# Performance work log

Hardware: AMD Instinct MI355X
Metric: run time of the kernel (lower is better)

Reference implementation:

```python
import jax, jax.numpy as jnp
import numpy as np

N_EVENTS = 16
N_SAMPLES = 2 ** 15          # 32768
STEP = 256                   # window_size // 2
LONG_WINDOW = 4096
LONG_COEFFS = LONG_WINDOW // 2 + 1   # 2049
LONG_STEP = LONG_WINDOW // 2         # 2048
LONG_FRAMES = N_SAMPLES // LONG_STEP # 16
N_FRAMES = N_SAMPLES // STEP         # 128
B = 8                                 # audio batch
BE = B * N_EVENTS                     # event batch = 128


def setup_inputs() -> dict:
    key = jax.random.key(0)
    k1, k2, k3, k4 = jax.random.split(key, 4)
    env = jax.random.uniform(k1, (BE, LONG_WINDOW, LONG_FRAMES), jnp.float32)
    tf = jax.random.normal(k2, (BE, LONG_COEFFS * 2, LONG_FRAMES), jnp.float32)
    noise = jax.random.uniform(k3, (BE, LONG_WINDOW, LONG_FRAMES), jnp.float32)
    indices = jax.random.randint(k4, (B, N_EVENTS), 0, N_FRAMES, dtype=jnp.int32)
    return {"env": env, "tf": tf, "noise": noise, "indices": indices}


def _event_render(env, tf, noise):
    # env, noise: (BE, LONG_WINDOW, LONG_FRAMES); tf: (BE, 2*LONG_COEFFS, LONG_FRAMES)
    batch = env.shape[0]
    energy = env * (noise * 2.0 - 1.0)  # uniform_(-1, 1) noise scaled by amp

    # magnitude = norm over interleaved (real, imag) pairs, per torch view semantics
    pairs = tf.reshape(batch, LONG_COEFFS, 2, LONG_FRAMES)
    mag = jnp.sqrt(jnp.sum(pairs * pairs, axis=2))  # (batch, C, F)
    mx = jnp.max(mag.reshape(batch, -1), axis=-1, keepdims=True)
    mag = (mag.reshape(batch, -1) / (mx + 1e-8)).reshape(batch, LONG_COEFFS, LONG_FRAMES)
    imag = tf[:, LONG_COEFFS:, :]
    phase = jnp.arctan2(imag, mag) * np.pi  # torch.angle(complex(mag, imag)) * pi
    tfc = mag * jnp.exp(1j * phase)         # complex transfer fn (batch, C, F)

    # sequential per-frame recurrence: state feeds through rfft/irfft filtering
    e_t = jnp.transpose(energy, (2, 0, 1))  # (F, batch, W)
    t_t = jnp.transpose(tfc, (2, 0, 1))     # (F, batch, C)

    def step(prev, inp):
        e, t = inp
        local = prev + e
        spec = jnp.fft.rfft(local, axis=-1, norm='ortho') * t
        frame = jnp.fft.irfft(spec, n=LONG_WINDOW, axis=-1, norm='ortho')
        return frame, frame

    init = jnp.zeros((batch, LONG_WINDOW), energy.dtype)
    _, frames = jax.lax.scan(step, init, (e_t, t_t))   # (F, batch, W)
    frames = jnp.transpose(frames, (1, 0, 2))          # (batch, F, W)

    # overlap-add with hop = LONG_STEP = W/2: split frames into halves and add
    halves = frames.reshape(batch, LONG_FRAMES, 2, LONG_STEP)
    out = jnp.zeros((batch, LONG_FRAMES + 1, LONG_STEP), frames.dtype)
    out = out.at[:, :LONG_FRAMES].add(halves[:, :, 0])
    out = out.at[:, 1:].add(halves[:, :, 1])
    return out.reshape(batch, -1)[:, :N_SAMPLES]       # (BE, N_SAMPLES)


def _segment_render(atoms, indices):
    # atoms: (BE, N_SAMPLES) -> (B, N_EVENTS, N_SAMPLES); scatter-add at time offsets
    x = atoms.reshape(B, N_EVENTS, N_SAMPLES)
    times = indices * STEP                                      # (B, E)
    pos = times[:, :, None] + jnp.arange(N_SAMPLES)[None, None, :]  # (B, E, S)
    out = jnp.zeros((B, 2 * N_SAMPLES), x.dtype)
    bidx = jnp.arange(B)[:, None, None]
    out = out.at[bidx, pos].add(x)
    return out[:, None, :N_SAMPLES]                             # (B, 1, N_SAMPLES)


def reference(env, tf, noise, indices):
    atoms = _event_render(env, tf, noise)
    return _segment_render(atoms, indices)
```

## Files before the change

### kernel.cpp

```cpp
#include <hip/hip_runtime.h>
#include <math.h>

#define TWO_PI 6.283185307179586f

#define OFF_ET   0ull
#define OFF_E    8388608ull
#define OFF_MAXP 16781312ull
#define OFF_Z    16782336ull

__device__ __forceinline__ int swz(int n) { return n ^ ((n >> 5) & 31); }

__device__ __forceinline__ int permf(int k) {
    return ((k & 1) << 10) | (((k >> 1) & 3) << 8) | (((k >> 3) & 3) << 6)
         | (((k >> 5) & 3) << 4) | (((k >> 7) & 3) << 2) | ((k >> 9) & 3);
}

__device__ __forceinline__ void r4f_core(float* cr, float* ci, int p0, int p1, int p2, int p3,
                                         float c1, float s1, float c2, float s2, float c3, float s3) {
    float ar = cr[p0], ai = ci[p0];
    float br = cr[p1], bi = ci[p1];
    float crr = cr[p2], cri = ci[p2];
    float drr = cr[p3], dri = ci[p3];
    float u0r = ar + crr, u0i = ai + cri;
    float u1r = ar - crr, u1i = ai - cri;
    float u2r = br + drr, u2i = bi + dri;
    float u3r = br - drr, u3i = bi - dri;
    cr[p0] = u0r + u2r; ci[p0] = u0i + u2i;
    float z1r = u1r + u3i, z1i = u1i - u3r;
    cr[p1] = z1r * c1 + z1i * s1; ci[p1] = z1i * c1 - z1r * s1;
    float z2r = u0r - u2r, z2i = u0i - u2i;
    cr[p2] = z2r * c2 + z2i * s2; ci[p2] = z2i * c2 - z2r * s2;
    float z3r = u1r - u3i, z3i = u1i + u3r;
    cr[p3] = z3r * c3 + z3i * s3; ci[p3] = z3i * c3 - z3r * s3;
}

__device__ __forceinline__ void r4i_core(float* cr, float* ci, int p0, int p1, int p2, int p3,
                                         float c1, float s1, float c2, float s2, float c3, float s3) {
    float z0r = cr[p0], z0i = ci[p0];
    float z1r = cr[p1], z1i = ci[p1];
    float z2r = cr[p2], z2i = ci[p2];
    float z3r = cr[p3], z3i = ci[p3];
    float t1r = z1r * c1 - z1i * s1, t1i = z1i * c1 + z1r * s1;
    float t2r = z2r * c2 - z2i * s2, t2i = z2i * c2 + z2r * s2;
    float t3r = z3r * c3 - z3i * s3, t3i = z3i * c3 + z3r * s3;
    float u0r = z0r + t2r, u0i = z0i + t2i;
    float u1r = z0r - t2r, u1i = z0i - t2i;
    float u2r = t1r + t3r, u2i = t1i + t3i;
    float u3r = t1r - t3r, u3i = t1i - t3i;
    cr[p0] = u0r + u2r; ci[p0] = u0i + u2i;
    cr[p1] = u1r - u3i; ci[p1] = u1i + u3r;
    cr[p2] = u0r - u2r; ci[p2] = u0i - u2i;
    cr[p3] = u1r + u3i; ci[p3] = u1i - u3r;
}

#define STAGE4(CORE, JEXPR, H, ANG)                                            \
    {                                                                          \
        int j_ = (JEXPR);                                                      \
        int p0 = swz(j_), p1 = swz(j_ + (H)), p2 = swz(j_ + 2 * (H)),          \
            p3 = swz(j_ + 3 * (H));                                            \
        float s1, c1; __sincosf((ANG), &s1, &c1);                              \
        float c2 = c1 * c1 - s1 * s1, s2 = 2.f * c1 * s1;                      \
        float c3 = c1 * c2 - s1 * s2, s3 = s1 * c2 + c1 * s2;                  \
        CORE(B + 0,     B + 2048,  p0, p1, p2, p3, c1, s1, c2, s2, c3, s3);    \
        CORE(B + 4096,  B + 6144,  p0, p1, p2, p3, c1, s1, c2, s2, c3, s3);    \
        CORE(B + 8192,  B + 10240, p0, p1, p2, p3, c1, s1, c2, s2, c3, s3);    \
        CORE(B + 12288, B + 14336, p0, p1, p2, p3, c1, s1, c2, s2, c3, s3);    \
    }                                                                          \
    __syncthreads();

__global__ __launch_bounds__(512, 4) void k_fwd(const float* __restrict__ env,
                                                const float* __restrict__ noise,
                                                const float* __restrict__ tf,
                                                float* __restrict__ ws) {
    __shared__ float B[16384];
    int tid = threadIdx.x;
    int id = blockIdx.x;
    if (id < 512) {
        int xcd = id & 7, slot = id >> 3;
        int be = xcd * 16 + (slot >> 2);
        int fg = slot & 3;
        const float4* env4 = (const float4*)env;
        const float4* noi4 = (const float4*)noise;
        size_t base = (size_t)be * 16384 + fg;
        for (int it = 0; it < 8; ++it) {
            int n = it * 512 + tid;
            float4 e = env4[base + (size_t)n * 4];
            float4 z = noi4[base + (size_t)n * 4];
            float v0 = e.x * (z.x * 2.0f - 1.0f);
            float v1 = e.y * (z.y * 2.0f - 1.0f);
            float v2 = e.z * (z.z * 2.0f - 1.0f);
            float v3 = e.w * (z.w * 2.0f - 1.0f);
            int m = swz(n >> 1) + (n & 1) * 2048;
            B[m] = v0; B[4096 + m] = v1; B[8192 + m] = v2; B[12288 + m] = v3;
        }
        __syncthreads();
#pragma unroll
        for (int it = 0; it < 2; ++it) {
            int i = tid + it * 512;
            int sj = swz(i), sjb = swz(i + 1024);
            float s, c; __sincosf((float)i * (TWO_PI / 2048.0f), &s, &c);
#pragma unroll
            for (int j4 = 0; j4 < 4; ++j4) {
                float* cr = B + j4 * 4096;
                float* ci = cr + 2048;
                float ar = cr[sj], ai = ci[sj], br = cr[sjb], bi = ci[sjb];
                float dr = ar - br, di = ai - bi;
                cr[sj] = ar + br; ci[sj] = ai + bi;
                cr[sjb] = dr * c + di * s; ci[sjb] = di * c - dr * s;
            }
        }
        __syncthreads();
        STAGE4(r4f_core, (tid >> 8) * 1024 + (tid & 255), 256, (float)(tid & 255) * (TWO_PI / 1024.0f));
        STAGE4(r4f_core, (tid >> 6) * 256 + (tid & 63), 64, (float)(tid & 63) * (TWO_PI / 256.0f));
        STAGE4(r4f_core, (tid & 31) * 64 + (tid >> 5), 16, (float)(tid >> 5) * (TWO_PI / 64.0f));
        STAGE4(r4f_core, (tid & 127) * 16 + (tid >> 7), 4, (float)(tid >> 7) * (TWO_PI / 16.0f));
        STAGE4(r4f_core, tid * 4, 1, 0.0f);
        float2* Ebase = (float2*)(ws + OFF_E) + (size_t)(be * 16 + fg * 4) * 2049;
        for (int it = 0; it < 3; ++it) {
            int k = tid + it * 512;
            if (k <= 1024) {
                int pk = swz(permf(k));
                int pm = swz(permf((2048 - k) & 2047));
                float s4, c4; __sincosf((float)k * (TWO_PI / 4096.0f), &s4, &c4);
#pragma unroll
                for (int j4 = 0; j4 < 4; ++j4) {
                    float* cr = B + j4 * 4096;
                    float* ci = cr + 2048;
                    float zkr = cr[pk], zki = ci[pk], zmr = cr[pm], zmi = ci[pm];
                    float xer = 0.5f * (zkr + zmr), xei = 0.5f * (zki - zmi);
                    float xor_ = 0.5f * (zki + zmi), xoi = 0.5f * (zmr - zkr);
                    float wr = xor_ * c4 + xoi * s4;
                    float wi = xoi * c4 - xor_ * s4;
                    float2* Eg = Ebase + (size_t)j4 * 2049;
                    Eg[k] = make_float2(xer + wr, xei + wi);
                    Eg[2048 - k] = make_float2(xer - wr, wi - xei);
                }
            }
        }
    } else {
        int bb = id - 512;
        int be = bb >> 1, c = bb & 1;
        const float4* ab4 = (const float4*)(tf + (size_t)be * 65568);
        float mx = 0.f;
        int start = c * 4098, end = start + 4098;
        for (int u = start + tid; u < end; u += 512) {
            int bin = u >> 2, e = u & 3;
            float4 A = ab4[bin * 8 + e];
            float4 Bv = ab4[bin * 8 + e + 4];
            mx = fmaxf(mx, fmaxf(fmaxf(A.x * A.x + Bv.x * Bv.x, A.y * A.y + Bv.y * Bv.y),
                                 fmaxf(A.z * A.z + Bv.z * Bv.z, A.w * A.w + Bv.w * Bv.w)));
        }
        B[tid] = mx;
        __syncthreads();
        for (int s = 256; s > 0; s >>= 1) {
            if (tid < s) B[tid] = fmaxf(B[tid], B[tid + s]);
            __syncthreads();
        }
        if (tid == 0) ws[OFF_MAXP + bb] = B[0];
    }
}

__global__ __launch_bounds__(256) void k_recur(const float* __restrict__ tf,
                                               float* __restrict__ ws) {
    __shared__ float sm2lo[256 * 17], simlo[256 * 17];
    __shared__ float sm2hi[256 * 17], simhi[256 * 17];
    int tid = threadIdx.x;
    int be = blockIdx.y;
    int k0 = blockIdx.x << 8;
    int hi0 = 1793 - k0;
    const float* tfb = tf + (size_t)be * 65568;
    const float4* ab4 = (const float4*)tfb;
    const float4* im4 = (const float4*)(tfb + 32784);

    for (int u = tid; u < 2048; u += 256) {
        int half = u >> 10, v = u & 1023;
        int g = v >> 2, e = v & 3;
        int bin = half ? (hi0 + g) : (k0 + g);
        float4 A = ab4[bin * 8 + e];
        float4 Bv = ab4[bin * 8 + e + 4];
        float4 I = im4[bin * 4 + e];
        int o = g * 17 + e * 4;
        float* sm = half ? sm2hi : sm2lo;
        float* si = half ? simhi : simlo;
        sm[o + 0] = A.x * A.x + Bv.x * Bv.x;
        sm[o + 1] = A.y * A.y + Bv.y * Bv.y;
        sm[o + 2] = A.z * A.z + Bv.z * Bv.z;
        sm[o + 3] = A.w * A.w + Bv.w * Bv.w;
        si[o + 0] = I.x; si[o + 1] = I.y; si[o + 2] = I.z; si[o + 3] = I.w;
    }
    __syncthreads();

    int k = k0 + tid;
    int m = 2048 - k;
    int rhi = 255 - tid;
    const float* mp = ws + OFF_MAXP + be * 2;
    float m2x = fmaxf(mp[0], mp[1]);
    float rden = 1.0f / (sqrtf(m2x) + 1e-8f);
    const float2* Eb = (const float2*)(ws + OFF_E) + (size_t)be * 16 * 2049;
    float2* Zb = (float2*)(ws + OFF_Z) + (size_t)be * 16 * 2048;
    float2 evlo[16], evhi[16];
#pragma unroll
    for (int f = 0; f < 16; ++f) {
        evlo[f] = Eb[(size_t)f * 2049 + k];
        evhi[f] = Eb[(size_t)f * 2049 + m];
    }
    float ym = (k == 0) ? 0.0f : 1.0f;
    float s4, c4; __sincosf((float)k * (TWO_PI / 4096.0f), &s4, &c4);
    const float SCL = 1.0f / 2048.0f;
    float srl = 0.f, sil = 0.f, srh = 0.f, sih = 0.f;
#pragma unroll
    for (int f = 0; f < 16; ++f) {
        float mh = sqrtf(sm2lo[tid * 17 + f]) * rden;
        float ph = atan2f(simlo[tid * 17 + f], mh) * 3.14159265358979f;
        float sp, cp; __sincosf(ph, &sp, &cp);
        float Tr = mh * cp, Ti = mh * sp;
        sil *= ym;
        srl += evlo[f].x; sil += evlo[f].y;
        float nr = srl * Tr - sil * Ti;
        sil = srl * Ti + sil * Tr; srl = nr;
        float mh2 = sqrtf(sm2hi[rhi * 17 + f]) * rden;
        float ph2 = atan2f(simhi[rhi * 17 + f], mh2) * 3.14159265358979f;
        float sp2, cp2; __sincosf(ph2, &sp2, &cp2);
        float Tr2 = mh2 * cp2, Ti2 = mh2 * sp2;
        sih *= ym;
        srh += evhi[f].x; sih += evhi[f].y;
        float nr2 = srh * Tr2 - sih * Ti2;
        sih = srh * Ti2 + sih * Tr2; srh = nr2;
        float2* Zf = Zb + (size_t)f * 2048;
        if (k == 0) {
            float y0 = srl * SCL, yn = srh * SCL;
            Zf[0] = make_float2(0.5f * (y0 + yn), 0.5f * (y0 - yn));
        } else {
            float ykr = srl * SCL, yki = sil * SCL;
            float ymr = srh * SCL, ymi = sih * SCL;
            float er = 0.5f * (ykr + ymr), ei = 0.5f * (yki - ymi);
            float dr = ykr - ymr, di = yki + ymi;
            float orr = 0.5f * (dr * c4 - di * s4);
            float oi = 0.5f * (dr * s4 + di * c4);
            Zf[k] = make_float2(er - oi, ei + orr);
            Zf[m] = make_float2(er + oi, orr - ei);
        }
    }
    if (k0 == 0 && tid == 0) {
        float sr = 0.f, si = 0.f;
#pragma unroll
        for (int f = 0; f < 16; ++f) {
            float a = tfb[1024 * 32 + f];
            float b = tfb[1024 * 32 + 16 + f];
            float im = tfb[32784 + 1024 * 16 + f];
            float mh = sqrtf(a * a + b * b) * rden;
            float ph = atan2f(im, mh) * 3.14159265358979f;
            float sp, cp; __sincosf(ph, &sp, &cp);
            float Tr = mh * cp, Ti = mh * sp;
            float2 e = Eb[(size_t)f * 2049 + 1024];
            sr += e.x; si += e.y;
            float nr = sr * Tr - si * Ti;
            si = sr * Ti + si * Tr; sr = nr;
            Zb[(size_t)f * 2048 + 1024] = make_float2(sr * SCL, -si * SCL);
        }
    }
}

__global__ __launch_bounds__(512, 4) void k_fft_inv(float* __restrict__ ws) {
    __shared__ float B[16384];
    int tid = threadIdx.x;
    int be = blockIdx.x >> 2, fg = blockIdx.x & 3;
    const float2* Zbase = (const float2*)(ws + OFF_Z) + (size_t)(be * 16 + fg * 4) * 2048;
#pragma unroll
    for (int j4 = 0; j4 < 4; ++j4) {
        const float4* Zg = (const float4*)(Zbase + (size_t)j4 * 2048);
        float* cr = B + j4 * 4096;
        float* ci = cr + 2048;
#pragma unroll
        for (int it = 0; it < 2; ++it) {
            int idx = tid + it * 512;
            float4 v = Zg[idx];
            int n0 = idx * 2;
            int p0 = swz(permf(n0)), p1 = swz(permf(n0 + 1));
            cr[p0] = v.x; ci[p0] = v.y;
            cr[p1] = v.z; ci[p1] = v.w;
        }
    }
    __syncthreads();
    STAGE4(r4i_core, tid * 4, 1, 0.0f);
    STAGE4(r4i_core, (tid & 127) * 16 + (tid >> 7), 4, (float)(tid >> 7) * (TWO_PI / 16.0f));
    STAGE4(r4i_core, (tid & 31) * 64 + (tid >> 5), 16, (float)(tid >> 5) * (TWO_PI / 64.0f));
    STAGE4(r4i_core, (tid >> 6) * 256 + (tid & 63), 64, (float)(tid & 63) * (TWO_PI / 256.0f));
    STAGE4(r4i_core, (tid >> 8) * 1024 + (tid & 255), 256, (float)(tid & 255) * (TWO_PI / 1024.0f));
#pragma unroll
    for (int it = 0; it < 2; ++it) {
        int i = tid + it * 512;
        int sj = swz(i), sjb = swz(i + 1024);
        float s, c; __sincosf((float)i * (TWO_PI / 2048.0f), &s, &c);
#pragma unroll
        for (int j4 = 0; j4 < 4; ++j4) {
            float* cr = B + j4 * 4096;
            float* ci = cr + 2048;
            float br = cr[sjb], bi = ci[sjb];
            float tr = br * c - bi * s, ti2 = br * s + bi * c;
            float ar = cr[sj], ai = ci[sj];
            cr[sj] = ar + tr;  ci[sj] = ai + ti2;
            cr[sjb] = ar - tr; ci[sjb] = ai - ti2;
        }
    }
    __syncthreads();
    float2* Fbase = (float2*)(ws + OFF_ET) + (size_t)(be * 16 + fg * 4) * 2048;
#pragma unroll
    for (int j4 = 0; j4 < 4; ++j4) {
        float* cr = B + j4 * 4096;
        float* ci = cr + 2048;
        float2* Fg = Fbase + (size_t)j4 * 2048;
#pragma unroll
        for (int it = 0; it < 4; ++it) {
            int m = tid + it * 512;
            Fg[m] = make_float2(cr[swz(m)], ci[swz(m)]);
        }
    }
}

__global__ __launch_bounds__(256) void k_segment(const float* __restrict__ ws,
                                                 const int* __restrict__ indices,
                                                 float* __restrict__ out) {
    __shared__ int ste[16];
    int tid = threadIdx.x;
    int b = blockIdx.y;
    if (tid < 16) ste[tid] = indices[b * 16 + tid] * 256;
    __syncthreads();
    int g = blockIdx.x * 256 + tid;
    int t = g << 2;
    const float* F = ws + OFF_ET;
    float4 acc = make_float4(0.f, 0.f, 0.f, 0.f);
#pragma unroll
    for (int e = 0; e < 16; ++e) {
        int te = ste[e];
        if (t >= te) {
            int d = t - te;
            int j = d >> 11, r = d & 2047;
            size_t base = (size_t)(b * 16 + e) * 65536;
            float4 v = *(const float4*)(F + base + j * 4096 + r);
            acc.x += v.x; acc.y += v.y; acc.z += v.z; acc.w += v.w;
            if (j >= 1) {
                float4 w = *(const float4*)(F + base + (j - 1) * 4096 + 2048 + r);
                acc.x += w.x; acc.y += w.y; acc.z += w.z; acc.w += w.w;
            }
        }
    }
    ((float4*)out)[(size_t)b * 8192 + g] = acc;
}

extern "C" void kernel_launch(void* const* d_in, const int* in_sizes, int n_in,
                              void* d_out, int out_size, void* d_ws, size_t ws_size,
                              hipStream_t stream) {
    const float* env = (const float*)d_in[0];
    const float* tf = (const float*)d_in[1];
    const float* noise = (const float*)d_in[2];
    const int* indices = (const int*)d_in[3];
    float* ws = (float*)d_ws;
    float* out = (float*)d_out;

    k_fwd<<<dim3(768), dim3(512), 0, stream>>>(env, noise, tf, ws);
    k_recur<<<dim3(4, 128), dim3(256), 0, stream>>>(tf, ws);
    k_fft_inv<<<dim3(512), dim3(512), 0, stream>>>(ws);
    k_segment<<<dim3(32, 8), dim3(256), 0, stream>>>(ws, indices, out);
}
```

Before: 83.15 us.

## Halve per-block FFT batch to double block count and occupancy

Forward and inverse FFT kernels now process 2 frames per block instead of 4, halving shared memory to 32KB and doubling the grid to 1024 blocks with launch bounds allowing 8 blocks per CU. Each thread now handles two butterflies per stage across the two frames. The separate magnitude-max blocks are folded into every forward block, with each block computing a partial max over its slice of bins; the recurrence kernel reduces 8 partials instead of 2. The aim is more parallelism and latency hiding, at the cost of more blocks, smaller float2 global loads, and a max reduction that now runs after the FFT in every block.

```diff
diff --git a/kernel.cpp b/kernel.cpp
--- a/kernel.cpp
+++ b/kernel.cpp
@@ -53,111 +53,114 @@
     cr[p3] = u1r + u3i; ci[p3] = u1i - u3r;
 }
 
-#define STAGE4(CORE, JEXPR, H, ANG)                                            \
+#define STAGE2X(CORE, JEXPR, H, ANGEXPR)                                       \
     {                                                                          \
-        int j_ = (JEXPR);                                                      \
-        int p0 = swz(j_), p1 = swz(j_ + (H)), p2 = swz(j_ + 2 * (H)),          \
-            p3 = swz(j_ + 3 * (H));                                            \
-        float s1, c1; __sincosf((ANG), &s1, &c1);                              \
-        float c2 = c1 * c1 - s1 * s1, s2 = 2.f * c1 * s1;                      \
-        float c3 = c1 * c2 - s1 * s2, s3 = s1 * c2 + c1 * s2;                  \
-        CORE(B + 0,     B + 2048,  p0, p1, p2, p3, c1, s1, c2, s2, c3, s3);    \
-        CORE(B + 4096,  B + 6144,  p0, p1, p2, p3, c1, s1, c2, s2, c3, s3);    \
-        CORE(B + 8192,  B + 10240, p0, p1, p2, p3, c1, s1, c2, s2, c3, s3);    \
-        CORE(B + 12288, B + 14336, p0, p1, p2, p3, c1, s1, c2, s2, c3, s3);    \
+        _Pragma("unroll")                                                      \
+        for (int half_ = 0; half_ < 2; ++half_) {                              \
+            int b_ = tid + half_ * 512;                                        \
+            int i_ = b_ & 511;                                                 \
+            float* cr_ = B + (b_ >> 9) * 4096;                                 \
+            float* ci_ = cr_ + 2048;                                           \
+            int j_ = (JEXPR);                                                  \
+            int p0 = swz(j_), p1 = swz(j_ + (H)), p2 = swz(j_ + 2 * (H)),      \
+                p3 = swz(j_ + 3 * (H));                                        \
+            float s1, c1; __sincosf((ANGEXPR), &s1, &c1);                      \
+            float c2 = c1 * c1 - s1 * s1, s2 = 2.f * c1 * s1;                  \
+            float c3 = c1 * c2 - s1 * s2, s3 = s1 * c2 + c1 * s2;              \
+            CORE(cr_, ci_, p0, p1, p2, p3, c1, s1, c2, s2, c3, s3);            \
+        }                                                                      \
     }                                                                          \
     __syncthreads();
 
-__global__ __launch_bounds__(512, 4) void k_fwd(const float* __restrict__ env,
+__global__ __launch_bounds__(512, 8) void k_fwd(const float* __restrict__ env,
                                                 const float* __restrict__ noise,
                                                 const float* __restrict__ tf,
                                                 float* __restrict__ ws) {
-    __shared__ float B[16384];
+    __shared__ float B[8192];
     int tid = threadIdx.x;
     int id = blockIdx.x;
-    if (id < 512) {
-        int xcd = id & 7, slot = id >> 3;
-        int be = xcd * 16 + (slot >> 2);
-        int fg = slot & 3;
-        const float4* env4 = (const float4*)env;
-        const float4* noi4 = (const float4*)noise;
-        size_t base = (size_t)be * 16384 + fg;
-        for (int it = 0; it < 8; ++it) {
-            int n = it * 512 + tid;
-            float4 e = env4[base + (size_t)n * 4];
-            float4 z = noi4[base + (size_t)n * 4];
-            float v0 = e.x * (z.x * 2.0f - 1.0f);
-            float v1 = e.y * (z.y * 2.0f - 1.0f);
-            float v2 = e.z * (z.z * 2.0f - 1.0f);
-            float v3 = e.w * (z.w * 2.0f - 1.0f);
-            int m = swz(n >> 1) + (n & 1) * 2048;
-            B[m] = v0; B[4096 + m] = v1; B[8192 + m] = v2; B[12288 + m] = v3;
-        }
+    int xcd = id & 7, slot = id >> 3;
+    int be = xcd * 16 + (slot >> 3);
+    int fg = slot & 7;
+    const float2* env2 = (const float2*)env;
+    const float2* noi2 = (const float2*)noise;
+    size_t base = (size_t)be * 32768 + fg;
+
+#pragma unroll
+    for (int it = 0; it < 8; ++it) {
+        int n = tid + it * 512;
+        float2 e = env2[base + (size_t)n * 8];
+        float2 z = noi2[base + (size_t)n * 8];
+        float v0 = e.x * (z.x * 2.0f - 1.0f);
+        float v1 = e.y * (z.y * 2.0f - 1.0f);
+        int m = (n & 1) * 2048 + swz(n >> 1);
+        B[m] = v0; B[4096 + m] = v1;
+    }
+    __syncthreads();
+#pragma unroll
+    for (int it = 0; it < 2; ++it) {
+        int i = tid + it * 512;
+        int sj = swz(i), sjb = swz(i + 1024);
+        float s, c; __sincosf((float)i * (TWO_PI / 2048.0f), &s, &c);
+#pragma unroll
+        for (int j2 = 0; j2 < 2; ++j2) {
+            float* cr = B + j2 * 4096;
+            float* ci = cr + 2048;
+            float ar = cr[sj], ai = ci[sj], br = cr[sjb], bi = ci[sjb];
+            float dr = ar - br, di = ai - bi;
+            cr[sj] = ar + br; ci[sj] = ai + bi;
+            cr[sjb] = dr * c + di * s; ci[sjb] = di * c - dr * s;
+        }
+    }
+    __syncthreads();
+    STAGE2X(r4f_core, (i_ >> 8) * 1024 + (i_ & 255), 256, (float)(i_ & 255) * (TWO_PI / 1024.0f));
+    STAGE2X(r4f_core, (i_ >> 6) * 256 + (i_ & 63), 64, (float)(i_ & 63) * (TWO_PI / 256.0f));
+    STAGE2X(r4f_core, (i_ & 31) * 64 + (i_ >> 5), 16, (float)(i_ >> 5) * (TWO_PI / 64.0f));
+    STAGE2X(r4f_core, (i_ & 127) * 16 + (i_ >> 7), 4, (float)(i_ >> 7) * (TWO_PI / 16.0f));
+    STAGE2X(r4f_core, i_ * 4, 1, 0.0f);
+    float2* Ebase = (float2*)(ws + OFF_E) + (size_t)(be * 16 + fg * 2) * 2049;
+#pragma unroll
+    for (int it = 0; it < 3; ++it) {
+        int k = tid + it * 512;
+        if (k <= 1024) {
+            int pk = swz(permf(k));
+            int pm = swz(permf((2048 - k) & 2047));
+            float s4, c4; __sincosf((float)k * (TWO_PI / 4096.0f), &s4, &c4);
+#pragma unroll
+            for (int j2 = 0; j2 < 2; ++j2) {
+                float* cr = B + j2 * 4096;
+                float* ci = cr + 2048;
+                float zkr = cr[pk], zki = ci[pk], zmr = cr[pm], zmi = ci[pm];
+                float xer = 0.5f * (zkr + zmr), xei = 0.5f * (zki - zmi);
+                float xor_ = 0.5f * (zki + zmi), xoi = 0.5f * (zmr - zkr);
+                float wr = xor_ * c4 + xoi * s4;
+                float wi = xoi * c4 - xor_ * s4;
+                float2* Eg = Ebase + (size_t)j2 * 2049;
+                Eg[k] = make_float2(xer + wr, xei + wi);
+                Eg[2048 - k] = make_float2(xer - wr, wi - xei);
+            }
+        }
+    }
+    __syncthreads();
+    const float4* ab4 = (const float4*)(tf + (size_t)be * 65568);
+    int b0 = fg * 257;
+    int nb = (fg == 7) ? 250 : 257;
+    float mx = 0.f;
+    for (int u = tid; u < nb * 4; u += 512) {
+        int g = u >> 2, e = u & 3;
+        int bin = b0 + g;
+        float4 A = ab4[bin * 8 + e];
+        float4 Bv = ab4[bin * 8 + e + 4];
+        mx = fmaxf(mx, fmaxf(fmaxf(A.x * A.x + Bv.x * Bv.x, A.y * A.y + Bv.y * Bv.y),
+                             fmaxf(A.z * A.z + Bv.z * Bv.z, A.w * A.w + Bv.w * Bv.w)));
+    }
+    B[tid] = mx;
+    __syncthreads();
+    for (int s = 256; s > 0; s >>= 1) {
+        if (tid < s) B[tid] = fmaxf(B[tid], B[tid + s]);
         __syncthreads();
-#pragma unroll
-        for (int it = 0; it < 2; ++it) {
-            int i = tid + it * 512;
-            int sj = swz(i), sjb = swz(i + 1024);
-            float s, c; __sincosf((float)i * (TWO_PI / 2048.0f), &s, &c);
-#pragma unroll
-            for (int j4 = 0; j4 < 4; ++j4) {
-                float* cr = B + j4 * 4096;
-                float* ci = cr + 2048;
-                float ar = cr[sj], ai = ci[sj], br = cr[sjb], bi = ci[sjb];
-                float dr = ar - br, di = ai - bi;
-                cr[sj] = ar + br; ci[sj] = ai + bi;
-                cr[sjb] = dr * c + di * s; ci[sjb] = di * c - dr * s;
-            }
-        }
-        __syncthreads();
-        STAGE4(r4f_core, (tid >> 8) * 1024 + (tid & 255), 256, (float)(tid & 255) * (TWO_PI / 1024.0f));
-        STAGE4(r4f_core, (tid >> 6) * 256 + (tid & 63), 64, (float)(tid & 63) * (TWO_PI / 256.0f));
-        STAGE4(r4f_core, (tid & 31) * 64 + (tid >> 5), 16, (float)(tid >> 5) * (TWO_PI / 64.0f));
-        STAGE4(r4f_core, (tid & 127) * 16 + (tid >> 7), 4, (float)(tid >> 7) * (TWO_PI / 16.0f));
-        STAGE4(r4f_core, tid * 4, 1, 0.0f);
-        float2* Ebase = (float2*)(ws + OFF_E) + (size_t)(be * 16 + fg * 4) * 2049;
-        for (int it = 0; it < 3; ++it) {
-            int k = tid + it * 512;
-            if (k <= 1024) {
-                int pk = swz(permf(k));
-                int pm = swz(permf((2048 - k) & 2047));
-                float s4, c4; __sincosf((float)k * (TWO_PI / 4096.0f), &s4, &c4);
-#pragma unroll
-                for (int j4 = 0; j4 < 4; ++j4) {
-                    float* cr = B + j4 * 4096;
-                    float* ci = cr + 2048;
-                    float zkr = cr[pk], zki = ci[pk], zmr = cr[pm], zmi = ci[pm];
-                    float xer = 0.5f * (zkr + zmr), xei = 0.5f * (zki - zmi);
-                    float xor_ = 0.5f * (zki + zmi), xoi = 0.5f * (zmr - zkr);
-                    float wr = xor_ * c4 + xoi * s4;
-                    float wi = xoi * c4 - xor_ * s4;
-                    float2* Eg = Ebase + (size_t)j4 * 2049;
-                    Eg[k] = make_float2(xer + wr, xei + wi);
-                    Eg[2048 - k] = make_float2(xer - wr, wi - xei);
-                }
-            }
-        }
-    } else {
-        int bb = id - 512;
-        int be = bb >> 1, c = bb & 1;
-        const float4* ab4 = (const float4*)(tf + (size_t)be * 65568);
-        float mx = 0.f;
-        int start = c * 4098, end = start + 4098;
-        for (int u = start + tid; u < end; u += 512) {
-            int bin = u >> 2, e = u & 3;
-            float4 A = ab4[bin * 8 + e];
-            float4 Bv = ab4[bin * 8 + e + 4];
-            mx = fmaxf(mx, fmaxf(fmaxf(A.x * A.x + Bv.x * Bv.x, A.y * A.y + Bv.y * Bv.y),
-                                 fmaxf(A.z * A.z + Bv.z * Bv.z, A.w * A.w + Bv.w * Bv.w)));
-        }
-        B[tid] = mx;
-        __syncthreads();
-        for (int s = 256; s > 0; s >>= 1) {
-            if (tid < s) B[tid] = fmaxf(B[tid], B[tid + s]);
-            __syncthreads();
-        }
-        if (tid == 0) ws[OFF_MAXP + bb] = B[0];
-    }
+    }
+    if (tid == 0) ws[OFF_MAXP + be * 8 + fg] = B[0];
 }
 
 __global__ __launch_bounds__(256) void k_recur(const float* __restrict__ tf,
@@ -193,8 +196,9 @@
     int k = k0 + tid;
     int m = 2048 - k;
     int rhi = 255 - tid;
-    const float* mp = ws + OFF_MAXP + be * 2;
-    float m2x = fmaxf(mp[0], mp[1]);
+    const float* mp = ws + OFF_MAXP + be * 8;
+    float m2x = fmaxf(fmaxf(fmaxf(mp[0], mp[1]), fmaxf(mp[2], mp[3])),
+                      fmaxf(fmaxf(mp[4], mp[5]), fmaxf(mp[6], mp[7])));
     float rden = 1.0f / (sqrtf(m2x) + 1e-8f);
     const float2* Eb = (const float2*)(ws + OFF_E) + (size_t)be * 16 * 2049;
     float2* Zb = (float2*)(ws + OFF_Z) + (size_t)be * 16 * 2048;
@@ -261,40 +265,39 @@
     }
 }
 
-__global__ __launch_bounds__(512, 4) void k_fft_inv(float* __restrict__ ws) {
-    __shared__ float B[16384];
+__global__ __launch_bounds__(512, 8) void k_fft_inv(float* __restrict__ ws) {
+    __shared__ float B[8192];
     int tid = threadIdx.x;
-    int be = blockIdx.x >> 2, fg = blockIdx.x & 3;
-    const float2* Zbase = (const float2*)(ws + OFF_Z) + (size_t)(be * 16 + fg * 4) * 2048;
-#pragma unroll
-    for (int j4 = 0; j4 < 4; ++j4) {
-        const float4* Zg = (const float4*)(Zbase + (size_t)j4 * 2048);
-        float* cr = B + j4 * 4096;
-        float* ci = cr + 2048;
-#pragma unroll
-        for (int it = 0; it < 2; ++it) {
-            int idx = tid + it * 512;
-            float4 v = Zg[idx];
-            int n0 = idx * 2;
-            int p0 = swz(permf(n0)), p1 = swz(permf(n0 + 1));
+    int be = blockIdx.x >> 3, fg = blockIdx.x & 7;
+    const float2* Zbase = (const float2*)(ws + OFF_Z) + (size_t)(be * 16 + fg * 2) * 2048;
+#pragma unroll
+    for (int it = 0; it < 2; ++it) {
+        int idx = tid + it * 512;
+        int n0 = idx * 2;
+        int p0 = swz(permf(n0)), p1 = swz(permf(n0 + 1));
+#pragma unroll
+        for (int j2 = 0; j2 < 2; ++j2) {
+            float4 v = ((const float4*)(Zbase + (size_t)j2 * 2048))[idx];
+            float* cr = B + j2 * 4096;
+            float* ci = cr + 2048;
             cr[p0] = v.x; ci[p0] = v.y;
             cr[p1] = v.z; ci[p1] = v.w;
         }
     }
     __syncthreads();
-    STAGE4(r4i_core, tid * 4, 1, 0.0f);
-    STAGE4(r4i_core, (tid & 127) * 16 + (tid >> 7), 4, (float)(tid >> 7) * (TWO_PI / 16.0f));
-    STAGE4(r4i_core, (tid & 31) * 64 + (tid >> 5), 16, (float)(tid >> 5) * (TWO_PI / 64.0f));
-    STAGE4(r4i_core, (tid >> 6) * 256 + (tid & 63), 64, (float)(tid & 63) * (TWO_PI / 256.0f));
-    STAGE4(r4i_core, (tid >> 8) * 1024 + (tid & 255), 256, (float)(tid & 255) * (TWO_PI / 1024.0f));
+    STAGE2X(r4i_core, i_ * 4, 1, 0.0f);
+    STAGE2X(r4i_core, (i_ & 127) * 16 + (i_ >> 7), 4, (float)(i_ >> 7) * (TWO_PI / 16.0f));
+    STAGE2X(r4i_core, (i_ & 31) * 64 + (i_ >> 5), 16, (float)(i_ >> 5) * (TWO_PI / 64.0f));
+    STAGE2X(r4i_core, (i_ >> 6) * 256 + (i_ & 63), 64, (float)(i_ & 63) * (TWO_PI / 256.0f));
+    STAGE2X(r4i_core, (i_ >> 8) * 1024 + (i_ & 255), 256, (float)(i_ & 255) * (TWO_PI / 1024.0f));
 #pragma unroll
     for (int it = 0; it < 2; ++it) {
         int i = tid + it * 512;
         int sj = swz(i), sjb = swz(i + 1024);
         float s, c; __sincosf((float)i * (TWO_PI / 2048.0f), &s, &c);
 #pragma unroll
-        for (int j4 = 0; j4 < 4; ++j4) {
-            float* cr = B + j4 * 4096;
+        for (int j2 = 0; j2 < 2; ++j2) {
+            float* cr = B + j2 * 4096;
             float* ci = cr + 2048;
             float br = cr[sjb], bi = ci[sjb];
             float tr = br * c - bi * s, ti2 = br * s + bi * c;
@@ -304,12 +307,12 @@
         }
     }
     __syncthreads();
-    float2* Fbase = (float2*)(ws + OFF_ET) + (size_t)(be * 16 + fg * 4) * 2048;
-#pragma unroll
-    for (int j4 = 0; j4 < 4; ++j4) {
-        float* cr = B + j4 * 4096;
+    float2* Fbase = (float2*)(ws + OFF_ET) + (size_t)(be * 16 + fg * 2) * 2048;
+#pragma unroll
+    for (int j2 = 0; j2 < 2; ++j2) {
+        float* cr = B + j2 * 4096;
         float* ci = cr + 2048;
-        float2* Fg = Fbase + (size_t)j4 * 2048;
+        float2* Fg = Fbase + (size_t)j2 * 2048;
 #pragma unroll
         for (int it = 0; it < 4; ++it) {
             int m = tid + it * 512;
@@ -358,8 +361,8 @@
     float* ws = (float*)d_ws;
     float* out = (float*)d_out;
 
-    k_fwd<<<dim3(768), dim3(512), 0, stream>>>(env, noise, tf, ws);
+    k_fwd<<<dim3(1024), dim3(512), 0, stream>>>(env, noise, tf, ws);
     k_recur<<<dim3(4, 128), dim3(256), 0, stream>>>(tf, ws);
-    k_fft_inv<<<dim3(512), dim3(512), 0, stream>>>(ws);
+    k_fft_inv<<<dim3(1024), dim3(512), 0, stream>>>(ws);
     k_segment<<<dim3(32, 8), dim3(256), 0, stream>>>(ws, indices, out);
 }
```

Result: slower. 86.92 us (+4.5%).
